# Kernel tuning notes

Measured on AMD Instinct MI355X. Metric: run time of the kernel, lower is better.

The kernel has to match this reference:

```python
import jax, jax.numpy as jnp
import numpy as np

K = 16          # neighbors per center (init arg K)
EPS = 1e-5      # layernorm epsilon


def _dcconv(pos, ch, W, b, n_in, n_out, resnet_in=None, Wres=None, bres=None):
    """KNN-gathered distance-contained conv.
    pos: [B, n_in, 3], ch: [B, n_in, Cin], W: [Cout, K, Cin].
    Selects n_out strided centers, gathers K nearest neighbors, convolves.
    """
    stride = n_in // n_out
    idx = jnp.arange(n_out) * stride                      # static center indices
    cpos = pos[:, idx]                                    # [B, n_out, 3]
    # squared pairwise distances centers -> all points: [B, n_out, n_in]
    d2 = jnp.sum((cpos[:, :, None, :] - pos[:, None, :, :]) ** 2, axis=-1)
    _, knn = jax.lax.top_k(-d2, K)                        # [B, n_out, K]
    gathered = jax.vmap(lambda c, i: c[i])(ch, knn)       # [B, n_out, K, Cin]
    out = jnp.einsum('bnkc,okc->bno', gathered, W) + b    # [B, n_out, Cout]
    if resnet_in is None:
        res = ch[:, idx] @ Wres + bres                    # project skip to Cout
    else:
        res = resnet_in[:, idx]                           # downsample carried skip
    return cpos, out, res


def _layernorm(x, g, b):
    mu = jnp.mean(x, axis=-1, keepdims=True)
    var = jnp.var(x, axis=-1, keepdims=True)
    return (x - mu) * jax.lax.rsqrt(var + EPS) * g + b


def setup_inputs() -> dict:
    key = jax.random.key(0)
    ks = jax.random.split(key, 8)
    B, N, Cin, Cout = 2, 8192, 64, 128
    s1 = (2.0 / (K * Cin)) ** 0.5
    s2 = (2.0 / (K * Cout)) ** 0.5
    return {
        'position_matrix': jax.random.normal(ks[0], (B, N, 3), jnp.float32),
        'channel_matrix': jax.random.normal(ks[1], (B, N, Cin), jnp.float32),
        'W1': jax.random.normal(ks[2], (Cout, K, Cin), jnp.float32) * s1,
        'b1': jnp.full((Cout,), 0.01, jnp.float32),
        'Wres': jax.random.normal(ks[3], (Cin, Cout), jnp.float32) * (2.0 / Cin) ** 0.5,
        'bres': jnp.full((Cout,), 0.01, jnp.float32),
        'W2': jax.random.normal(ks[4], (Cout, K, Cout), jnp.float32) * s2,
        'b2': jnp.full((Cout,), 0.01, jnp.float32),
        'g1': jnp.ones((Cout,), jnp.float32),
        'be1': jnp.full((Cout,), 0.01, jnp.float32),
        'g2': jnp.ones((Cout,), jnp.float32),
        'be2': jnp.full((Cout,), 0.01, jnp.float32),
        'n0': 8192, 'n1': 4096, 'n2': 2048,
    }


def reference(position_matrix, channel_matrix, W1, b1, Wres, bres, W2, b2,
              g1, be1, g2, be2, n0, n1, n2):
    pos, ch, res = _dcconv(position_matrix, channel_matrix, W1, b1, n0, n1,
                           None, Wres, bres)
    ch = jax.nn.silu(_layernorm(ch, g1, be1))   # dropout=identity (eval)
    pos, ch, res = _dcconv(pos, ch, W2, b2, n1, n2, resnet_in=res)
    ch = jax.nn.silu(_layernorm(ch, g2, be2))   # dropout=identity (eval)
    ch = ch + res                               # residual add
    return pos, ch
```

## Files before the change

### kernel.cpp

```cpp
#include <hip/hip_runtime.h>
#include <cstdint>
#include <cstddef>

using u16 = unsigned short;
using u32 = unsigned int;
using u64 = unsigned long long;

typedef short bf16x8 __attribute__((ext_vector_type(8)));
typedef float f32x4 __attribute__((ext_vector_type(4)));
typedef float f4a __attribute__((ext_vector_type(4), aligned(4)));
typedef float f2a __attribute__((ext_vector_type(2), aligned(4)));

constexpr int N0 = 8192;
constexpr int N1 = 4096;
constexpr int N2 = 2048;
constexpr int COUT = 128;
constexpr int KNB = 16;

__device__ __forceinline__ float bf2f(u16 v) { return __uint_as_float(((u32)v) << 16); }
__device__ __forceinline__ u16 f2bf(float f) {
    u32 u = __float_as_uint(f);
    return (u16)((u + 0x7fffu + ((u >> 16) & 1u)) >> 16);
}
__device__ __forceinline__ void cvt8(const float* __restrict__ src, u16* __restrict__ dst, int e) {
    float t0[8];
    *(float4*)t0 = *(const float4*)(src + e);
    *(float4*)(t0 + 4) = *(const float4*)(src + e + 4);
    u16 o[8];
#pragma unroll
    for (int q = 0; q < 8; ++q) o[q] = f2bf(t0[q]);
    *(uint4*)(dst + e) = *(uint4*)o;
}

__device__ __forceinline__ float dist2s(float cx, float cy, float cz,
                                        float px, float py, float pz) {
#pragma clang fp contract(off)
    float dx = cx - px;
    float dy = cy - py;
    float dz = cz - pz;
    float s = dx * dx;
    s = s + dy * dy;
    s = s + dz * dz;
    return s;
}

template <int CTRL>
__device__ __forceinline__ u64 dpp64(u64 v) {
    int lo = (int)(u32)v, hi = (int)(u32)(v >> 32);
    int plo = __builtin_amdgcn_update_dpp(0, lo, CTRL, 0xF, 0xF, true);
    int phi = __builtin_amdgcn_update_dpp(0, hi, CTRL, 0xF, 0xF, true);
    return (((u64)(u32)phi) << 32) | (u32)plo;
}
__device__ __forceinline__ u64 dpp_prev_u64(u64 v) { return dpp64<0x111>(v); }

__device__ __forceinline__ u32 rdlane(u32 v, int l) {
    return (u32)__builtin_amdgcn_readlane((int)v, l);
}

template <int PSTRIDE>
__device__ __forceinline__ void knn_scan(const float* __restrict__ P,
                                         int c0row, int c1row, int cnt,
                                         int lane, u64& rk0, u64& rk1) {
    const float* c0p = P + (size_t)c0row * PSTRIDE;
    const float* c1p = P + (size_t)c1row * PSTRIDE;
    float c0x = c0p[0], c0y = c0p[1], c0z = c0p[2];
    float c1x = c1p[0], c1y = c1p[1], c1z = c1p[2];

    u64 key0, key1;
    {
        const float* pp = P + (size_t)lane * PSTRIDE;
        float px = pp[0], py = pp[1], pz = pp[2];
        u64 k0 = (((u64)__float_as_uint(dist2s(c0x, c0y, c0z, px, py, pz))) << 32) | (u32)lane;
        u64 k1 = (((u64)__float_as_uint(dist2s(c1x, c1y, c1z, px, py, pz))) << 32) | (u32)lane;
#pragma unroll
        for (int kk = 2; kk <= 64; kk <<= 1)
#pragma unroll
            for (int jj = kk >> 1; jj > 0; jj >>= 1) {
                u64 o0, o1;
                if (jj == 1)      { o0 = dpp64<0xB1>(k0);  o1 = dpp64<0xB1>(k1); }
                else if (jj == 2) { o0 = dpp64<0x4E>(k0);  o1 = dpp64<0x4E>(k1); }
                else if (jj == 8) { o0 = dpp64<0x128>(k0); o1 = dpp64<0x128>(k1); }
                else              { o0 = __shfl_xor(k0, jj, 64); o1 = __shfl_xor(k1, jj, 64); }
                bool keepmin = (((lane & jj) == 0) == ((lane & kk) == 0));
                k0 = keepmin ? ((o0 < k0) ? o0 : k0) : ((o0 > k0) ? o0 : k0);
                k1 = keepmin ? ((o1 < k1) ? o1 : k1) : ((o1 > k1) ? o1 : k1);
            }
        key0 = k0; key1 = k1;
    }
    u32 cut0 = rdlane((u32)(key0 >> 32), 15);
    u32 cut1 = rdlane((u32)(key1 >> 32), 15);

    {
        const float* pp = P + (size_t)(64 + lane) * PSTRIDE;
        float px = pp[0], py = pp[1], pz = pp[2];
        u32 d0 = __float_as_uint(dist2s(c0x, c0y, c0z, px, py, pz));
        u32 d1 = __float_as_uint(dist2s(c1x, c1y, c1z, px, py, pz));
        u64 ball0 = __ballot(d0 <= cut0);
        u64 ball1 = __ballot(d1 <= cut1);
        bool any0 = ball0 != 0, any1 = ball1 != 0;
        while (ball0 | ball1) {
            if (ball0) {
                int src = __ffsll((unsigned long long)ball0) - 1;
                ball0 &= ball0 - 1;
                u64 nk = (((u64)rdlane(d0, src)) << 32) | (u32)(64 + src);
                u64 prev = dpp_prev_u64(key0);
                key0 = (nk < key0) ? ((nk < prev) ? prev : nk) : key0;
            }
            if (ball1) {
                int src = __ffsll((unsigned long long)ball1) - 1;
                ball1 &= ball1 - 1;
                u64 nk = (((u64)rdlane(d1, src)) << 32) | (u32)(64 + src);
                u64 prev = dpp_prev_u64(key1);
                key1 = (nk < key1) ? ((nk < prev) ? prev : nk) : key1;
            }
        }
        if (any0) cut0 = rdlane((u32)(key0 >> 32), 15);
        if (any1) cut1 = rdlane((u32)(key1 >> 32), 15);
    }

    constexpr int STEPF = 128 * PSTRIDE;
    int nstep = (cnt - 128) >> 7;
    const float* cur = P + (size_t)(128 + 2 * lane) * PSTRIDE;
    f4a va; f4a vb;
    if constexpr (PSTRIDE == 3) {
        va = *(const f4a*)cur;
        f2a t = *(const f2a*)(cur + 4);
        vb.x = t.x; vb.y = t.y;
    } else {
        va = *(const f4a*)cur;
        vb = *(const f4a*)(cur + 5);
    }
    for (int s = 0; s < nstep; ++s) {
        float cax, cay, caz, cbx, cby, cbz;
        if constexpr (PSTRIDE == 3) {
            cax = va.x; cay = va.y; caz = va.z;
            cbx = va.w; cby = vb.x; cbz = vb.y;
        } else {
            cax = va.x; cay = va.y; caz = va.z;
            cbx = vb.y; cby = vb.z; cbz = vb.w;
        }
        cur += STEPF;
        if (s + 1 < nstep) {
            if constexpr (PSTRIDE == 3) {
                va = *(const f4a*)cur;
                f2a t = *(const f2a*)(cur + 4);
                vb.x = t.x; vb.y = t.y;
            } else {
                va = *(const f4a*)cur;
                vb = *(const f4a*)(cur + 5);
            }
        }
        int sb = 128 + (s << 7);
        u32 da0 = __float_as_uint(dist2s(c0x, c0y, c0z, cax, cay, caz));
        u32 da1 = __float_as_uint(dist2s(c1x, c1y, c1z, cax, cay, caz));
        u32 db0 = __float_as_uint(dist2s(c0x, c0y, c0z, cbx, cby, cbz));
        u32 db1 = __float_as_uint(dist2s(c1x, c1y, c1z, cbx, cby, cbz));
        u64 ba0 = __ballot(da0 <= cut0);
        u64 bb0 = __ballot(db0 <= cut0);
        u64 ba1 = __ballot(da1 <= cut1);
        u64 bb1 = __ballot(db1 <= cut1);
        bool any0 = (ba0 | bb0) != 0, any1 = (ba1 | bb1) != 0;
        while (ba0 | bb0 | ba1 | bb1) {
            if (ba0) {
                int src = __ffsll((unsigned long long)ba0) - 1;
                ba0 &= ba0 - 1;
                u64 nk = (((u64)rdlane(da0, src)) << 32) | (u32)(sb + 2 * src);
                u64 prev = dpp_prev_u64(key0);
                key0 = (nk < key0) ? ((nk < prev) ? prev : nk) : key0;
            }
            if (ba1) {
                int src = __ffsll((unsigned long long)ba1) - 1;
                ba1 &= ba1 - 1;
                u64 nk = (((u64)rdlane(da1, src)) << 32) | (u32)(sb + 2 * src);
                u64 prev = dpp_prev_u64(key1);
                key1 = (nk < key1) ? ((nk < prev) ? prev : nk) : key1;
            }
            if (bb0) {
                int src = __ffsll((unsigned long long)bb0) - 1;
                bb0 &= bb0 - 1;
                u64 nk = (((u64)rdlane(db0, src)) << 32) | (u32)(sb + 2 * src + 1);
                u64 prev = dpp_prev_u64(key0);
                key0 = (nk < key0) ? ((nk < prev) ? prev : nk) : key0;
            }
            if (bb1) {
                int src = __ffsll((unsigned long long)bb1) - 1;
                bb1 &= bb1 - 1;
                u64 nk = (((u64)rdlane(db1, src)) << 32) | (u32)(sb + 2 * src + 1);
                u64 prev = dpp_prev_u64(key1);
                key1 = (nk < key1) ? ((nk < prev) ? prev : nk) : key1;
            }
        }
        if (any0) cut0 = rdlane((u32)(key0 >> 32), 15);
        if (any1) cut1 = rdlane((u32)(key1 >> 32), 15);
    }
    rk0 = key0; rk1 = key1;
}

__global__ __launch_bounds__(256)
void knn_prep_kernel(const float* __restrict__ pos0, const float* __restrict__ ch0,
                     const float* __restrict__ W1, const float* __restrict__ W2,
                     const float* __restrict__ Wres,
                     int* __restrict__ knn1, int* __restrict__ knn2,
                     u16* __restrict__ ch0b, u16* __restrict__ W1b,
                     u16* __restrict__ W2b, u16* __restrict__ Wresb,
                     float* __restrict__ pos_out) {
    int blk = blockIdx.x, tid = threadIdx.x;
    int w = tid >> 6, lane = tid & 63;
    if (blk < 1024) {
        int wave = blk * 4 + w;
        int batch = wave >> 11, pj = wave & 2047;
        const float* P = pos0 + (size_t)batch * N0 * 3;
        u64 key0, key1;
        knn_scan<3>(P, 4 * pj, 4 * pj + 2, N0, lane, key0, key1);
        if (lane < 16) {
            knn1[((size_t)(batch * N1 + 2 * pj)) * KNB + lane] = (int)(u32)key0;
            knn1[((size_t)(batch * N1 + 2 * pj + 1)) * KNB + lane] = (int)(u32)key1;
        }
    } else if (blk < 1536) {
        int wave = (blk - 1024) * 4 + w;
        int batch = wave >> 10, pj = wave & 1023;
        const float* P = pos0 + (size_t)batch * N0 * 3;
        u64 key0, key1;
        knn_scan<6>(P, 4 * pj, 4 * pj + 2, N1, lane, key0, key1);
        if (lane < 16) {
            knn2[((size_t)(batch * N2 + 2 * pj)) * KNB + lane] = (int)(u32)key0;
            knn2[((size_t)(batch * N2 + 2 * pj + 1)) * KNB + lane] = (int)(u32)key1;
        }
    } else if (blk < 2048) {
        cvt8(ch0, ch0b, ((blk - 1536) * 256 + tid) * 8);
    } else if (blk < 2112) {
        cvt8(W1, W1b, ((blk - 2048) * 256 + tid) * 8);
    } else if (blk < 2240) {
        cvt8(W2, W2b, ((blk - 2112) * 256 + tid) * 8);
    } else if (blk < 2272) {
        int t = (blk - 2240) * 256 + tid;
        int o = t >> 6, c = t & 63;
        Wresb[o * 64 + c] = f2bf(Wres[(size_t)c * COUT + o]);
    } else {
        int t = (blk - 2272) * 256 + tid;
        int b = t >> 11, r = t & 2047;
        const float* s = pos0 + ((size_t)(b * N0 + r * 4)) * 3;
        float* d = pos_out + ((size_t)(b * N2 + r)) * 3;
        d[0] = s[0]; d[1] = s[1]; d[2] = s[2];
    }
}

__global__ __launch_bounds__(512)
void conv1_kernel(const u16* __restrict__ ch0b, const int* __restrict__ knn1,
                  const u16* __restrict__ W1b, const u16* __restrict__ Wresb,
                  const float* __restrict__ b1, const float* __restrict__ bres,
                  const float* __restrict__ g1, const float* __restrict__ be1,
                  u16* __restrict__ ch1b, u16* __restrict__ res1b) {
    __shared__ u16 As[2][16][72];
    __shared__ int knnr[16][16];
    __shared__ float red[16][8][2];
    __shared__ float cb[128], cg[128], cbe[128], cbr[128];

    int blk = blockIdx.x, tid = threadIdx.x;
    int b = blk >> 8, g = blk & 255;
    int jbase = g * 16;

    if (tid < 128) { cb[tid] = b1[tid]; cg[tid] = g1[tid]; cbe[tid] = be1[tid]; cbr[tid] = bres[tid]; }
    if (tid < 256) {
        int r = tid >> 4, k = tid & 15;
        knnr[r][k] = knn1[((size_t)(b * N1 + jbase + r)) * KNB + k];
    }
    __syncthreads();

    int w = tid >> 6, lane = tid & 63, quad = lane >> 4, l15 = lane & 15;
    int wcol = w * 16;
    int ar = tid >> 5, ap = tid & 31;

    f32x4 acc = {0, 0, 0, 0};
    f32x4 racc = {0, 0, 0, 0};

    const u16* wbase = W1b + (size_t)(wcol + l15) * 1024 + quad * 8;

    u32 aR = *((const u32*)(ch0b + ((size_t)(b * N0 + knnr[ar][0])) * 64) + ap);
    uint4 wcur[2] = { *(const uint4*)wbase, *(const uint4*)(wbase + 32) };

    int pb = 0;
    for (int kn = 0; kn < 17; ++kn) {
        *(u32*)&As[pb][ar][ap * 2] = aR;
        __syncthreads();
        uint4 wnxt[2];
        if (kn < 16) {
            int nidx = (kn < 15) ? knnr[ar][kn + 1] : 2 * (jbase + ar);
            aR = *((const u32*)(ch0b + ((size_t)(b * N0 + nidx)) * 64) + ap);
            if (kn < 15) {
                const u16* p = wbase + (kn + 1) * 64;
                wnxt[0] = *(const uint4*)p; wnxt[1] = *(const uint4*)(p + 32);
            } else {
                const u16* p = Wresb + (size_t)(wcol + l15) * 64 + quad * 8;
                wnxt[0] = *(const uint4*)p; wnxt[1] = *(const uint4*)(p + 32);
            }
        }
        if (kn < 16) {
#pragma unroll
            for (int ks = 0; ks < 2; ++ks) {
                bf16x8 af = *(const bf16x8*)&As[pb][l15][ks * 32 + quad * 8];
                acc = __builtin_amdgcn_mfma_f32_16x16x32_bf16(af, *(const bf16x8*)&wcur[ks], acc, 0, 0, 0);
            }
        } else {
#pragma unroll
            for (int ks = 0; ks < 2; ++ks) {
                bf16x8 af = *(const bf16x8*)&As[pb][l15][ks * 32 + quad * 8];
                racc = __builtin_amdgcn_mfma_f32_16x16x32_bf16(af, *(const bf16x8*)&wcur[ks], racc, 0, 0, 0);
            }
        }
        if (kn < 16) { wcur[0] = wnxt[0]; wcur[1] = wnxt[1]; }
        pb ^= 1;
    }

    float x[4], s[4], ss[4];
#pragma unroll
    for (int reg = 0; reg < 4; ++reg) {
        int col = wcol + l15;
        float v = acc[reg] + cb[col];
        x[reg] = v; s[reg] = v; ss[reg] = v * v;
    }
#pragma unroll
    for (int m = 1; m < 16; m <<= 1)
#pragma unroll
        for (int reg = 0; reg < 4; ++reg) {
            s[reg] += __shfl_xor(s[reg], m, 64);
            ss[reg] += __shfl_xor(ss[reg], m, 64);
        }
    if (l15 == 0) {
#pragma unroll
        for (int reg = 0; reg < 4; ++reg) {
            red[quad * 4 + reg][w][0] = s[reg];
            red[quad * 4 + reg][w][1] = ss[reg];
        }
    }
    __syncthreads();
#pragma unroll
    for (int reg = 0; reg < 4; ++reg) {
        int row = quad * 4 + reg;
        float S = 0.f, SS = 0.f;
#pragma unroll
        for (int t = 0; t < 8; ++t) { S += red[row][t][0]; SS += red[row][t][1]; }
        float mu = S * (1.f / 128.f);
        float var = fmaxf(SS * (1.f / 128.f) - mu * mu, 0.f);
        float rs = 1.f / sqrtf(var + 1e-5f);
        int col = wcol + l15;
        size_t off = ((size_t)(b * N1 + jbase + row)) * COUT + col;
        float y = (x[reg] - mu) * rs * cg[col] + cbe[col];
        ch1b[off] = f2bf(y / (1.f + __expf(-y)));
        res1b[off] = f2bf(racc[reg] + cbr[col]);
    }
}

__global__ __launch_bounds__(512)
void conv2_kernel(const u16* __restrict__ ch1b, const int* __restrict__ knn2,
                  const u16* __restrict__ W2b, const float* __restrict__ b2,
                  const float* __restrict__ g2, const float* __restrict__ be2,
                  const u16* __restrict__ res1b, float* __restrict__ ch_out) {
    __shared__ u16 As[2][16][136];
    __shared__ int knnr[16][16];
    __shared__ float red[16][8][2];
    __shared__ float cb[128], cg[128], cbe[128];

    int tid = threadIdx.x;
    int b = blockIdx.x >> 7, g = blockIdx.x & 127;
    int ibase = g * 16;

    if (tid < 128) { cb[tid] = b2[tid]; cg[tid] = g2[tid]; cbe[tid] = be2[tid]; }
    if (tid < 256) {
        int r = tid >> 4, k = tid & 15;
        knnr[r][k] = knn2[((size_t)(b * N2 + ibase + r)) * KNB + k];
    }
    __syncthreads();

    int w = tid >> 6, lane = tid & 63, quad = lane >> 4, l15 = lane & 15;
    int wcol = w * 16;
    int ar = tid >> 5, ap = tid & 31;

    f32x4 acc = {0, 0, 0, 0};

    const u16* wbase = W2b + (size_t)(wcol + l15) * 2048 + quad * 8;

    uint2 aR = *((const uint2*)(ch1b + ((size_t)(b * N1 + knnr[ar][0])) * COUT) + ap);
    uint4 wcur[4] = { *(const uint4*)wbase, *(const uint4*)(wbase + 32),
                      *(const uint4*)(wbase + 64), *(const uint4*)(wbase + 96) };

    int pb = 0;
    for (int kn = 0; kn < 16; ++kn) {
        *(uint2*)&As[pb][ar][ap * 4] = aR;
        __syncthreads();
        uint4 wnxt[4];
        if (kn < 15) {
            aR = *((const uint2*)(ch1b + ((size_t)(b * N1 + knnr[ar][kn + 1])) * COUT) + ap);
            const u16* p = wbase + (kn + 1) * 128;
            wnxt[0] = *(const uint4*)p;        wnxt[1] = *(const uint4*)(p + 32);
            wnxt[2] = *(const uint4*)(p + 64); wnxt[3] = *(const uint4*)(p + 96);
        }
#pragma unroll
        for (int ks = 0; ks < 4; ++ks) {
            bf16x8 af = *(const bf16x8*)&As[pb][l15][ks * 32 + quad * 8];
            acc = __builtin_amdgcn_mfma_f32_16x16x32_bf16(af, *(const bf16x8*)&wcur[ks], acc, 0, 0, 0);
        }
        if (kn < 15) {
            wcur[0] = wnxt[0]; wcur[1] = wnxt[1]; wcur[2] = wnxt[2]; wcur[3] = wnxt[3];
        }
        pb ^= 1;
    }

    float x[4], s[4], ss[4];
#pragma unroll
    for (int reg = 0; reg < 4; ++reg) {
        int col = wcol + l15;
        float v = acc[reg] + cb[col];
        x[reg] = v; s[reg] = v; ss[reg] = v * v;
    }
#pragma unroll
    for (int m = 1; m < 16; m <<= 1)
#pragma unroll
        for (int reg = 0; reg < 4; ++reg) {
            s[reg] += __shfl_xor(s[reg], m, 64);
            ss[reg] += __shfl_xor(ss[reg], m, 64);
        }
    if (l15 == 0) {
#pragma unroll
        for (int reg = 0; reg < 4; ++reg) {
            red[quad * 4 + reg][w][0] = s[reg];
            red[quad * 4 + reg][w][1] = ss[reg];
        }
    }
    __syncthreads();
#pragma unroll
    for (int reg = 0; reg < 4; ++reg) {
        int row = quad * 4 + reg;
        float S = 0.f, SS = 0.f;
#pragma unroll
        for (int t = 0; t < 8; ++t) { S += red[row][t][0]; SS += red[row][t][1]; }
        float mu = S * (1.f / 128.f);
        float var = fmaxf(SS * (1.f / 128.f) - mu * mu, 0.f);
        float rs = 1.f / sqrtf(var + 1e-5f);
        int col = wcol + l15;
        int i = ibase + row;
        float y = (x[reg] - mu) * rs * cg[col] + cbe[col];
        float sl = y / (1.f + __expf(-y));
        float rv = bf2f(res1b[((size_t)(b * N1 + 2 * i)) * COUT + col]);
        ch_out[((size_t)(b * N2 + i)) * COUT + col] = sl + rv;
    }
}

extern "C" void kernel_launch(void* const* d_in, const int* in_sizes, int n_in,
                              void* d_out, int out_size, void* d_ws, size_t ws_size,
                              hipStream_t stream) {
    const float* pos0 = (const float*)d_in[0];
    const float* ch0  = (const float*)d_in[1];
    const float* W1   = (const float*)d_in[2];
    const float* b1   = (const float*)d_in[3];
    const float* Wres = (const float*)d_in[4];
    const float* bres = (const float*)d_in[5];
    const float* W2   = (const float*)d_in[6];
    const float* b2   = (const float*)d_in[7];
    const float* g1   = (const float*)d_in[8];
    const float* be1  = (const float*)d_in[9];
    const float* g2   = (const float*)d_in[10];
    const float* be2  = (const float*)d_in[11];
    float* out = (float*)d_out;

    char* ws = (char*)d_ws;
    int*  knn1  = (int*)(ws);
    int*  knn2  = (int*)(ws + 524288);
    u16*  ch0b  = (u16*)(ws + 786432);
    u16*  W1b   = (u16*)(ws + 2883584);
    u16*  W2b   = (u16*)(ws + 3145728);
    u16*  Wresb = (u16*)(ws + 3670016);
    u16*  ch1b  = (u16*)(ws + 3686400);
    u16*  res1b = (u16*)(ws + 5783552);

    float* pos_out = out;
    float* ch_out  = out + 12288;

    knn_prep_kernel<<<2288, 256, 0, stream>>>(pos0, ch0, W1, W2, Wres,
                                              knn1, knn2, ch0b, W1b, W2b, Wresb, pos_out);
    conv1_kernel<<<512, 512, 0, stream>>>(ch0b, knn1, W1b, Wresb, b1, bres, g1, be1,
                                          ch1b, res1b);
    conv2_kernel<<<256, 512, 0, stream>>>(ch1b, knn2, W2b, b2, g2, be2, res1b, ch_out);
}
```

Before: 183.1 us.

## Load gathered neighbor rows directly into MFMA registers, dropping LDS staging

Both conv kernels stop staging gathered neighbor rows in shared memory behind a per-neighbor __syncthreads. Each lane now loads its A fragment straight from global memory using the neighbor index, and the loop is unrolled by 4 so the compiler can keep several loads in flight. This removes 16-17 block barriers and the LDS round trip per block. In exchange every wave re-reads the same gathered rows from global/L2 (8 waves, so 8x redundant traffic), and the explicit software prefetch of weights is gone.

```diff
diff --git a/kernel.cpp b/kernel.cpp
--- a/kernel.cpp
+++ b/kernel.cpp
@@ -251,7 +251,6 @@
                   const float* __restrict__ b1, const float* __restrict__ bres,
                   const float* __restrict__ g1, const float* __restrict__ be1,
                   u16* __restrict__ ch1b, u16* __restrict__ res1b) {
-    __shared__ u16 As[2][16][72];
     __shared__ int knnr[16][16];
     __shared__ float red[16][8][2];
     __shared__ float cb[128], cg[128], cbe[128], cbr[128];
@@ -269,47 +268,30 @@
 
     int w = tid >> 6, lane = tid & 63, quad = lane >> 4, l15 = lane & 15;
     int wcol = w * 16;
-    int ar = tid >> 5, ap = tid & 31;
+
+    const u16* abase = ch0b + (size_t)b * N0 * 64 + quad * 8;
+    const u16* wbase = W1b + (size_t)(wcol + l15) * 1024 + quad * 8;
 
     f32x4 acc = {0, 0, 0, 0};
     f32x4 racc = {0, 0, 0, 0};
 
-    const u16* wbase = W1b + (size_t)(wcol + l15) * 1024 + quad * 8;
-
-    u32 aR = *((const u32*)(ch0b + ((size_t)(b * N0 + knnr[ar][0])) * 64) + ap);
-    uint4 wcur[2] = { *(const uint4*)wbase, *(const uint4*)(wbase + 32) };
-
-    int pb = 0;
-    for (int kn = 0; kn < 17; ++kn) {
-        *(u32*)&As[pb][ar][ap * 2] = aR;
-        __syncthreads();
-        uint4 wnxt[2];
-        if (kn < 16) {
-            int nidx = (kn < 15) ? knnr[ar][kn + 1] : 2 * (jbase + ar);
-            aR = *((const u32*)(ch0b + ((size_t)(b * N0 + nidx)) * 64) + ap);
-            if (kn < 15) {
-                const u16* p = wbase + (kn + 1) * 64;
-                wnxt[0] = *(const uint4*)p; wnxt[1] = *(const uint4*)(p + 32);
-            } else {
-                const u16* p = Wresb + (size_t)(wcol + l15) * 64 + quad * 8;
-                wnxt[0] = *(const uint4*)p; wnxt[1] = *(const uint4*)(p + 32);
-            }
-        }
-        if (kn < 16) {
-#pragma unroll
-            for (int ks = 0; ks < 2; ++ks) {
-                bf16x8 af = *(const bf16x8*)&As[pb][l15][ks * 32 + quad * 8];
-                acc = __builtin_amdgcn_mfma_f32_16x16x32_bf16(af, *(const bf16x8*)&wcur[ks], acc, 0, 0, 0);
-            }
-        } else {
-#pragma unroll
-            for (int ks = 0; ks < 2; ++ks) {
-                bf16x8 af = *(const bf16x8*)&As[pb][l15][ks * 32 + quad * 8];
-                racc = __builtin_amdgcn_mfma_f32_16x16x32_bf16(af, *(const bf16x8*)&wcur[ks], racc, 0, 0, 0);
-            }
-        }
-        if (kn < 16) { wcur[0] = wnxt[0]; wcur[1] = wnxt[1]; }
-        pb ^= 1;
+#pragma unroll 4
+    for (int kn = 0; kn < 16; ++kn) {
+        int row = knnr[l15][kn];
+        const u16* ap = abase + (size_t)row * 64;
+        const u16* wp = wbase + kn * 64;
+        bf16x8 a0 = *(const bf16x8*)ap;
+        bf16x8 a1 = *(const bf16x8*)(ap + 32);
+        acc = __builtin_amdgcn_mfma_f32_16x16x32_bf16(a0, *(const bf16x8*)wp, acc, 0, 0, 0);
+        acc = __builtin_amdgcn_mfma_f32_16x16x32_bf16(a1, *(const bf16x8*)(wp + 32), acc, 0, 0, 0);
+    }
+    {
+        const u16* ap = abase + (size_t)(2 * (jbase + l15)) * 64;
+        const u16* wp = Wresb + (size_t)(wcol + l15) * 64 + quad * 8;
+        bf16x8 a0 = *(const bf16x8*)ap;
+        bf16x8 a1 = *(const bf16x8*)(ap + 32);
+        racc = __builtin_amdgcn_mfma_f32_16x16x32_bf16(a0, *(const bf16x8*)wp, racc, 0, 0, 0);
+        racc = __builtin_amdgcn_mfma_f32_16x16x32_bf16(a1, *(const bf16x8*)(wp + 32), racc, 0, 0, 0);
     }
 
     float x[4], s[4], ss[4];
@@ -356,7 +338,6 @@
                   const u16* __restrict__ W2b, const float* __restrict__ b2,
                   const float* __restrict__ g2, const float* __restrict__ be2,
                   const u16* __restrict__ res1b, float* __restrict__ ch_out) {
-    __shared__ u16 As[2][16][136];
     __shared__ int knnr[16][16];
     __shared__ float red[16][8][2];
     __shared__ float cb[128], cg[128], cbe[128];
@@ -374,36 +355,23 @@
 
     int w = tid >> 6, lane = tid & 63, quad = lane >> 4, l15 = lane & 15;
     int wcol = w * 16;
-    int ar = tid >> 5, ap = tid & 31;
+
+    const u16* abase = ch1b + (size_t)b * N1 * 128 + quad * 8;
+    const u16* wbase = W2b + (size_t)(wcol + l15) * 2048 + quad * 8;
 
     f32x4 acc = {0, 0, 0, 0};
 
-    const u16* wbase = W2b + (size_t)(wcol + l15) * 2048 + quad * 8;
-
-    uint2 aR = *((const uint2*)(ch1b + ((size_t)(b * N1 + knnr[ar][0])) * COUT) + ap);
-    uint4 wcur[4] = { *(const uint4*)wbase, *(const uint4*)(wbase + 32),
-                      *(const uint4*)(wbase + 64), *(const uint4*)(wbase + 96) };
-
-    int pb = 0;
+#pragma unroll 4
     for (int kn = 0; kn < 16; ++kn) {
-        *(uint2*)&As[pb][ar][ap * 4] = aR;
-        __syncthreads();
-        uint4 wnxt[4];
-        if (kn < 15) {
-            aR = *((const uint2*)(ch1b + ((size_t)(b * N1 + knnr[ar][kn + 1])) * COUT) + ap);
-            const u16* p = wbase + (kn + 1) * 128;
-            wnxt[0] = *(const uint4*)p;        wnxt[1] = *(const uint4*)(p + 32);
-            wnxt[2] = *(const uint4*)(p + 64); wnxt[3] = *(const uint4*)(p + 96);
-        }
+        int row = knnr[l15][kn];
+        const u16* ap = abase + (size_t)row * 128;
+        const u16* wp = wbase + kn * 128;
 #pragma unroll
         for (int ks = 0; ks < 4; ++ks) {
-            bf16x8 af = *(const bf16x8*)&As[pb][l15][ks * 32 + quad * 8];
-            acc = __builtin_amdgcn_mfma_f32_16x16x32_bf16(af, *(const bf16x8*)&wcur[ks], acc, 0, 0, 0);
-        }
-        if (kn < 15) {
-            wcur[0] = wnxt[0]; wcur[1] = wnxt[1]; wcur[2] = wnxt[2]; wcur[3] = wnxt[3];
-        }
-        pb ^= 1;
+            acc = __builtin_amdgcn_mfma_f32_16x16x32_bf16(*(const bf16x8*)(ap + ks * 32),
+                                                          *(const bf16x8*)(wp + ks * 32),
+                                                          acc, 0, 0, 0);
+        }
     }
 
     float x[4], s[4], ss[4];
```

Result: slower. 208.5 us (+13.9%).
